# Kernel optimization log

Measured on AMD Instinct MI355X. Metric: run time of the kernel, lower is better.

Reference implementation:

```python
import jax, jax.numpy as jnp
import numpy as np

CLASSES, SIZE, INPUT_SIZE, CONTEXT_SIZE, BATCH = 8, 512, 512, 512, 64
CMS = 4          # context_map_size -> 2**CMS = 16 contexts per neuron
LR = 0.01
PRED_CLIP = 0.01
WEIGHT_CLIP = 5.0


def _logit(x):
    return jnp.log(x) - jnp.log1p(-x)


def setup_inputs() -> dict:
    key = jax.random.key(0)
    k1, k2, k3, k4, k5 = jax.random.split(key, 5)
    logits = jax.random.normal(k1, (CLASSES, INPUT_SIZE, BATCH), jnp.float32)
    context = jax.random.normal(k2, (BATCH, CONTEXT_SIZE), jnp.float32)
    target = jax.random.uniform(k3, (CLASSES, BATCH), jnp.float32)
    cmaps = jax.random.normal(k4, (CLASSES, SIZE, CMS, CONTEXT_SIZE), jnp.float32)
    cmaps = cmaps / jnp.linalg.norm(cmaps, axis=-1, keepdims=True)
    cbias = jax.random.normal(k5, (CLASSES, SIZE, CMS, 1), jnp.float32)
    weights = jnp.full((CLASSES, SIZE, 2 ** CMS, INPUT_SIZE), 1.0 / INPUT_SIZE, jnp.float32)
    return {"logits": logits, "context": context, "target": target,
            "context_maps": cmaps, "context_bias": cbias, "weights": weights}


def reference(logits, context, target, context_maps, context_bias, weights):
    # --- context hashing ---
    # distances: [classes, size, cms, batch]
    distances = jnp.einsum('cskd,bd->cskb', context_maps, context)
    bits = (distances > context_bias).astype(jnp.int32)
    conv = (2 ** jnp.arange(CMS, dtype=jnp.int32))[:, None]          # [cms, 1]
    idx = jnp.sum(bits * conv, axis=-2)                              # [classes, size, batch]
    # --- gather per-context weights ---
    c = jnp.arange(CLASSES)[:, None, None]
    s = jnp.arange(SIZE)[None, :, None]
    sel = weights[c, s, idx, :]                                      # [classes, size, batch, input]
    # --- per-sample dot product (== diagonal of the original batch x batch matmul) ---
    lo = _logit(jnp.float32(PRED_CLIP))
    hi = _logit(jnp.float32(1.0 - PRED_CLIP))
    out = jnp.clip(jnp.einsum('csbi,cib->csb', sel, logits), lo, hi)  # [classes, size, batch]
    # --- online weight update (clamped) scattered back ---
    sig = jax.nn.sigmoid(out)
    diff = sig - target[:, None, :]                                  # [classes, size, batch]
    # lr * diff[c,s,b] * logits[c,i,b]  -> update [c,s,b,i]
    upd = LR * diff[:, :, :, None] * jnp.transpose(logits, (0, 2, 1))[:, None, :, :]
    new_sel = jnp.clip(sel - upd, -WEIGHT_CLIP, WEIGHT_CLIP)
    new_weights = weights.at[c, s, idx, :].set(new_sel)
    return out, new_weights
```

## Files before the change

kernel.cpp:

```cpp
#include <hip/hip_runtime.h>
#include <math.h>

#define CLASSES 8
#define SIZE 512
#define ISZ 512
#define CSZ 512
#define BATCH 64
#define CMS 4
#define NBUCKET 16
#define LR 0.01f
#define WCLIP 5.0f
#define WSTRIDE 516

__global__ __launch_bounds__(256) void pack_pre(
    const float* __restrict__ logits,
    const float* __restrict__ context,
    float* __restrict__ Lt,
    float* __restrict__ Lpk,
    float* __restrict__ ctxT4)
{
    __shared__ float t[64][65];
    const int bid  = blockIdx.x;
    const int lane = threadIdx.x & 63;
    const int w    = threadIdx.x >> 6;
    if (bid < 64) {
        const int r0 = bid << 6;
        #pragma unroll
        for (int rep = 0; rep < 16; ++rep) {
            int rr = w * 16 + rep;
            t[rr][lane] = logits[(size_t)(r0 + rr) * 64 + lane];
        }
        __syncthreads();
        const int ci = r0 + lane;
        #pragma unroll
        for (int rep = 0; rep < 16; ++rep) {
            int b = w * 16 + rep;
            float v = t[lane][b];
            Lt[(size_t)b * 4096 + ci] = v;
            Lpk[(size_t)(ci >> 2) * 256 + 4 * b + (ci & 3)] = v;
        }
    } else {
        const int c0 = (bid - 64) << 6;
        #pragma unroll
        for (int rep = 0; rep < 16; ++rep) {
            int rr = w * 16 + rep;
            t[rr][lane] = context[(size_t)rr * 512 + c0 + lane];
        }
        __syncthreads();
        #pragma unroll
        for (int rep = 0; rep < 16; ++rep) {
            int dd = c0 + w * 16 + rep;
            ctxT4[(size_t)(dd >> 2) * 256 + 4 * lane + (dd & 3)] = t[lane][w * 16 + rep];
        }
    }
}

__global__ __launch_bounds__(256, 8) void dist_kernel(
    const float* __restrict__ cmaps,
    const float* __restrict__ cbias,
    const float* __restrict__ ctxT4,
    unsigned char* __restrict__ idxOut)
{
    __shared__ int bits[CMS * BATCH];

    const int tid  = threadIdx.x;
    const int cs   = blockIdx.x;
    const int lane = tid & 63;
    const int wv   = tid >> 6;
    const int k    = __builtin_amdgcn_readfirstlane(wv);

    const float4* cmg = (const float4*)(cmaps + ((size_t)cs * CMS + k) * CSZ);
    {
        const float4* ct4 = (const float4*)ctxT4 + lane;
        float acc = 0.f;
        #pragma unroll 4
        for (int d4 = 0; d4 < 128; ++d4) {
            float4 cm4 = cmg[d4];
            float4 cv  = ct4[(size_t)d4 * 64];
            acc += cm4.x * cv.x + cm4.y * cv.y + cm4.z * cv.z + cm4.w * cv.w;
        }
        float bias = cbias[(size_t)cs * CMS + k];
        bits[k * BATCH + lane] = (acc > bias) ? 1 : 0;
    }
    __syncthreads();

    if (wv == 0) {
        int idx_b = bits[lane] | (bits[BATCH + lane] << 1) |
                    (bits[2 * BATCH + lane] << 2) | (bits[3 * BATCH + lane] << 3);
        idxOut[(size_t)cs * BATCH + lane] = (unsigned char)idx_b;
    }
}

__global__ __launch_bounds__(256, 4) void gln_bc(
    const float* __restrict__ target,
    const float* __restrict__ weights,
    const unsigned char* __restrict__ idxIn,
    const float* __restrict__ Lt,
    const float* __restrict__ Lpk,
    float* __restrict__ out,
    float* __restrict__ outW)
{
    __shared__ float Wl[NBUCKET * WSTRIDE];
    __shared__ float partial[4 * BATCH];
    __shared__ float diff_l[BATCH];
    __shared__ int   blast[NBUCKET];

    const int tid  = threadIdx.x;
    const int cs   = blockIdx.x;
    const int c    = cs >> 9;
    const int lane = tid & 63;
    const int wv   = tid >> 6;

    float4 wreg[8];
    const float4* gW = (const float4*)(weights + (size_t)cs * (NBUCKET * ISZ));
    #pragma unroll
    for (int it = 0; it < 8; ++it) wreg[it] = gW[tid + it * 256];

    const int idx_b = idxIn[(size_t)cs * BATCH + lane];

    #pragma unroll
    for (int jj = 0; jj < 4; ++jj) {
        int j = (wv << 2) + jj;
        unsigned long long m = __ballot(idx_b == j);
        if (lane == 0) blast[j] = m ? (63 - __clzll(m)) : -1;
    }

    #pragma unroll
    for (int it = 0; it < 8; ++it) {
        int f = tid + it * 256;
        *(float4*)&Wl[(f >> 7) * WSTRIDE + (f & 127) * 4] = wreg[it];
    }
    __syncthreads();

    {
        const float4* Lp4 = (const float4*)Lpk;
        const int base4 = (c * 128 + wv * 32) * 64 + lane;
        const int wb    = idx_b * WSTRIDE + wv * 128;
        float acc = 0.f;
        #pragma unroll 4
        for (int d4 = 0; d4 < 32; ++d4) {
            float4 w4 = *(const float4*)&Wl[wb + d4 * 4];
            float4 l4 = Lp4[(size_t)base4 + d4 * 64];
            acc += w4.x * l4.x + w4.y * l4.y + w4.z * l4.z + w4.w * l4.w;
        }
        partial[wv * BATCH + lane] = acc;
    }
    __syncthreads();

    if (wv == 0) {
        float s = partial[lane] + partial[BATCH + lane] +
                  partial[2 * BATCH + lane] + partial[3 * BATCH + lane];
        const float hi = 4.595119850134589f;
        float oc = fminf(fmaxf(s, -hi), hi);
        out[(size_t)cs * BATCH + lane] = oc;
        float sig = 1.f / (1.f + expf(-oc));
        diff_l[lane] = LR * (sig - target[c * BATCH + lane]);
    }
    __syncthreads();

    float* gO = outW + (size_t)cs * (NBUCKET * ISZ);
    const float* LtC = Lt + (size_t)c * ISZ;
    #pragma unroll
    for (int it = 0; it < 8; ++it) {
        int f    = tid + it * 256;
        int row  = f >> 7;
        int col4 = f & 127;
        float4 w4 = wreg[it];
        int bl = blast[row];
        float4 r = w4;
        if (bl >= 0) {
            float coef = diff_l[bl];
            float4 l4  = ((const float4*)(LtC + (size_t)bl * 4096))[col4];
            r.x = fminf(fmaxf(w4.x - coef * l4.x, -WCLIP), WCLIP);
            r.y = fminf(fmaxf(w4.y - coef * l4.y, -WCLIP), WCLIP);
            r.z = fminf(fmaxf(w4.z - coef * l4.z, -WCLIP), WCLIP);
            r.w = fminf(fmaxf(w4.w - coef * l4.w, -WCLIP), WCLIP);
        }
        ((float4*)gO)[f] = r;
    }
}

extern "C" void kernel_launch(void* const* d_in, const int* in_sizes, int n_in,
                              void* d_out, int out_size, void* d_ws, size_t ws_size,
                              hipStream_t stream) {
    const float* logits  = (const float*)d_in[0];
    const float* context = (const float*)d_in[1];
    const float* target  = (const float*)d_in[2];
    const float* cmaps   = (const float*)d_in[3];
    const float* cbias   = (const float*)d_in[4];
    const float* weights = (const float*)d_in[5];

    float* out  = (float*)d_out;
    float* outW = out + (size_t)CLASSES * SIZE * BATCH;

    float* Lt    = (float*)d_ws;
    float* Lpk   = Lt + 262144;
    float* ctxT4 = Lpk + 262144;
    unsigned char* idxb = (unsigned char*)(ctxT4 + 32768);

    pack_pre<<<72, 256, 0, stream>>>(logits, context, Lt, Lpk, ctxT4);
    dist_kernel<<<CLASSES * SIZE, 256, 0, stream>>>(cmaps, cbias, ctxT4, idxb);
    gln_bc<<<CLASSES * SIZE, 256, 0, stream>>>(target, weights, idxb, Lt, Lpk, out, outW);
}
```

Baseline: 140.8 us.

## Split gather-dot and weight-update into two kernels via workspace

After: 158.5 us. +12.6%, slower.

```diff
diff --git a/kernel.cpp b/kernel.cpp
--- a/kernel.cpp
+++ b/kernel.cpp
@@ -91,19 +91,17 @@
     }
 }
 
-__global__ __launch_bounds__(256, 4) void gln_bc(
+__global__ __launch_bounds__(256, 4) void gln_bc1(
     const float* __restrict__ target,
     const float* __restrict__ weights,
     const unsigned char* __restrict__ idxIn,
-    const float* __restrict__ Lt,
     const float* __restrict__ Lpk,
     float* __restrict__ out,
-    float* __restrict__ outW)
+    float* __restrict__ diffW,
+    int*   __restrict__ blastW)
 {
     __shared__ float Wl[NBUCKET * WSTRIDE];
     __shared__ float partial[4 * BATCH];
-    __shared__ float diff_l[BATCH];
-    __shared__ int   blast[NBUCKET];
 
     const int tid  = threadIdx.x;
     const int cs   = blockIdx.x;
@@ -118,12 +116,14 @@
 
     const int idx_b = idxIn[(size_t)cs * BATCH + lane];
 
-    #pragma unroll
-    for (int jj = 0; jj < 4; ++jj) {
-        int j = (wv << 2) + jj;
+    int myblast = -1;
+    #pragma unroll
+    for (int j = 0; j < NBUCKET; ++j) {
         unsigned long long m = __ballot(idx_b == j);
-        if (lane == 0) blast[j] = m ? (63 - __clzll(m)) : -1;
-    }
+        int bl = m ? (63 - __clzll(m)) : -1;
+        if (lane == j) myblast = bl;
+    }
+    if (wv == 0 && lane < NBUCKET) blastW[cs * NBUCKET + lane] = myblast;
 
     #pragma unroll
     for (int it = 0; it < 8; ++it) {
@@ -154,29 +154,39 @@
         float oc = fminf(fmaxf(s, -hi), hi);
         out[(size_t)cs * BATCH + lane] = oc;
         float sig = 1.f / (1.f + expf(-oc));
-        diff_l[lane] = LR * (sig - target[c * BATCH + lane]);
-    }
-    __syncthreads();
-
-    float* gO = outW + (size_t)cs * (NBUCKET * ISZ);
-    const float* LtC = Lt + (size_t)c * ISZ;
-    #pragma unroll
-    for (int it = 0; it < 8; ++it) {
-        int f    = tid + it * 256;
-        int row  = f >> 7;
-        int col4 = f & 127;
-        float4 w4 = wreg[it];
-        int bl = blast[row];
+        diffW[(size_t)cs * BATCH + lane] = LR * (sig - target[c * BATCH + lane]);
+    }
+}
+
+__global__ __launch_bounds__(256) void gln_bc2(
+    const float* __restrict__ weights,
+    const float* __restrict__ Lt,
+    const float* __restrict__ diffW,
+    const int*   __restrict__ blastW,
+    float* __restrict__ outW)
+{
+    const int tid = threadIdx.x;
+    const float4* gW = (const float4*)weights;
+    float4* gO = (float4*)outW;
+    #pragma unroll
+    for (int it = 0; it < 4; ++it) {
+        size_t f = ((size_t)blockIdx.x * 4 + it) * 256 + tid;
+        int cs   = (int)(f >> 11);
+        int rw   = (int)(f >> 7) & 15;
+        int col4 = (int)f & 127;
+        int c    = cs >> 9;
+        float4 w4 = gW[f];
+        int bl = blastW[cs * NBUCKET + rw];
         float4 r = w4;
         if (bl >= 0) {
-            float coef = diff_l[bl];
-            float4 l4  = ((const float4*)(LtC + (size_t)bl * 4096))[col4];
+            float coef = diffW[(size_t)cs * BATCH + bl];
+            float4 l4  = ((const float4*)Lt)[(size_t)bl * 1024 + c * 128 + col4];
             r.x = fminf(fmaxf(w4.x - coef * l4.x, -WCLIP), WCLIP);
             r.y = fminf(fmaxf(w4.y - coef * l4.y, -WCLIP), WCLIP);
             r.z = fminf(fmaxf(w4.z - coef * l4.z, -WCLIP), WCLIP);
             r.w = fminf(fmaxf(w4.w - coef * l4.w, -WCLIP), WCLIP);
         }
-        ((float4*)gO)[f] = r;
+        gO[f] = r;
     }
 }
 
@@ -197,8 +207,11 @@
     float* Lpk   = Lt + 262144;
     float* ctxT4 = Lpk + 262144;
     unsigned char* idxb = (unsigned char*)(ctxT4 + 32768);
+    float* diffW = (float*)(idxb + 262144);
+    int*   blastW = (int*)(diffW + 262144);
 
     pack_pre<<<72, 256, 0, stream>>>(logits, context, Lt, Lpk, ctxT4);
     dist_kernel<<<CLASSES * SIZE, 256, 0, stream>>>(cmaps, cbias, ctxT4, idxb);
-    gln_bc<<<CLASSES * SIZE, 256, 0, stream>>>(target, weights, idxb, Lt, Lpk, out, outW);
-}
+    gln_bc1<<<CLASSES * SIZE, 256, 0, stream>>>(target, weights, idxb, Lpk, out, diffW, blastW);
+    gln_bc2<<<8192, 256, 0, stream>>>(weights, Lt, diffW, blastW, outW);
+}
```
